# Kernel optimization log

Hardware: AMD Instinct MI355X
Metric: run time of the kernel (lower is better)

## Reference

```python
import jax, jax.numpy as jnp
import numpy as np

N, B, FIN, E, EDIM, H, C = 20000, 2, 256, 320000, 64, 8, 32


def setup_inputs() -> dict:
    key = jax.random.key(0)
    ks = jax.random.split(key, 12)
    s = 1.0 / np.sqrt(FIN)
    se = 1.0 / np.sqrt(EDIM)
    return {
        "x": jax.random.normal(ks[0], (N, B, FIN), jnp.float32),
        "edata": jax.random.normal(ks[1], (E, EDIM), jnp.float32),
        "edge_src": jax.random.randint(ks[2], (E,), 0, N, jnp.int32),
        "edge_dst": jax.random.randint(ks[3], (E,), 0, N, jnp.int32),
        "Wq": jax.random.normal(ks[4], (FIN, H * C), jnp.float32) * s,
        "bq": jnp.zeros((H * C,), jnp.float32),
        "Wk": jax.random.normal(ks[5], (FIN, H * C), jnp.float32) * s,
        "bk": jnp.zeros((H * C,), jnp.float32),
        "Wv": jax.random.normal(ks[6], (FIN, H * C), jnp.float32) * s,
        "bv": jnp.zeros((H * C,), jnp.float32),
        "We": jax.random.normal(ks[7], (EDIM, H * C), jnp.float32) * se,
        "Wr": jax.random.normal(ks[8], (FIN, H * C), jnp.float32) * s,
        "br": jnp.zeros((H * C,), jnp.float32),
    }


def reference(x, edata, edge_src, edge_dst, Wq, bq, Wk, bk, Wv, bv, We, Wr, br):
    # x: [N, B, FIN]; edata: [E, EDIM]
    q = (x @ Wq + bq).reshape(N, B, H, C)   # dst queries
    k = (x @ Wk + bk).reshape(N, B, H, C)   # src keys
    v = (x @ Wv + bv).reshape(N, B, H, C)   # src values
    e = (edata @ We).reshape(E, 1, H, C)    # edge feats, broadcast over batch

    scale = 1.0 / np.sqrt(C)
    # per-edge logits: (u_mul_v / sqrt(C) + edata).sum(-1) -> [E, B, H]
    logits = (k[edge_src] * q[edge_dst] * scale + e).sum(-1)

    # edge_softmax over edges sharing the same destination node
    m = jax.ops.segment_max(logits, edge_dst, num_segments=N)      # [N, B, H]
    ex = jnp.exp(logits - m[edge_dst])
    z = jax.ops.segment_sum(ex, edge_dst, num_segments=N)          # [N, B, H]
    alpha = ex / z[edge_dst]                                       # [E, B, H]

    # weighted scatter-sum aggregation: u_mul_e + sum over dst
    att_v = v[edge_src] * alpha[..., None]                         # [E, B, H, C]
    agg = jax.ops.segment_sum(att_v, edge_dst, num_segments=N)     # [N, B, H, C]

    out = agg.reshape(N, B, H * C) + (x @ Wr + br)
    return out
```

## Files before the change

### kernel.cpp

```cpp
#include <hip/hip_runtime.h>
#include <hip/hip_bf16.h>

#define NN    20000
#define BB    2
#define EE    320000
#define MROWS (NN * BB)

typedef __bf16 bf16x8 __attribute__((ext_vector_type(8)));
typedef float  floatx4 __attribute__((ext_vector_type(4)));


__global__ __launch_bounds__(256) void transpose_weights(
    const float* __restrict__ Wq, const float* __restrict__ Wk,
    const float* __restrict__ Wv, const float* __restrict__ Wr,
    __hip_bfloat16* __restrict__ wt) {
  __shared__ float TA[32][65];
  __shared__ float TB[32][65];
  int bt = blockIdx.x;
  const float *A, *B;
  int c0, jbase;
  if (bt < 8) { A = Wk; B = Wv; c0 = 32 * bt;      jbase = 64 * bt; }
  else        { A = Wq; B = Wr; c0 = 32 * (bt-8);  jbase = 512 + 64 * (bt-8); }
  int t = threadIdx.x;
  int krow = t >> 2;
  int cc = (t & 3) * 8;
  int sel = t >> 7;
  int u = t & 127;
  int ci = u >> 2;
  int kk0 = (u & 3) * 16;

  for (int kt = 0; kt < 4; ++kt) {
    int k = kt * 64 + krow;
    float4 a0 = *(const float4*)(A + (size_t)k * 256 + c0 + cc);
    float4 a1 = *(const float4*)(A + (size_t)k * 256 + c0 + cc + 4);
    float4 b0 = *(const float4*)(B + (size_t)k * 256 + c0 + cc);
    float4 b1 = *(const float4*)(B + (size_t)k * 256 + c0 + cc + 4);
    __syncthreads();
    TA[cc+0][krow]=a0.x; TA[cc+1][krow]=a0.y; TA[cc+2][krow]=a0.z; TA[cc+3][krow]=a0.w;
    TA[cc+4][krow]=a1.x; TA[cc+5][krow]=a1.y; TA[cc+6][krow]=a1.z; TA[cc+7][krow]=a1.w;
    TB[cc+0][krow]=b0.x; TB[cc+1][krow]=b0.y; TB[cc+2][krow]=b0.z; TB[cc+3][krow]=b0.w;
    TB[cc+4][krow]=b1.x; TB[cc+5][krow]=b1.y; TB[cc+6][krow]=b1.z; TB[cc+7][krow]=b1.w;
    __syncthreads();
    float (*T)[65] = sel ? TB : TA;
    int j = jbase + 2 * ci + sel;
    __hip_bfloat16* dst = wt + (size_t)j * 256 + kt * 64 + kk0;
    #pragma unroll
    for (int q = 0; q < 16; ++q) dst[q] = __float2bfloat16(T[ci][kk0 + q]);
  }
}

__global__ void prep_bias(const float* __restrict__ bq, const float* __restrict__ bk,
                          const float* __restrict__ bv, const float* __restrict__ br,
                          float* __restrict__ bcat) {
  int j = blockIdx.x * 256 + threadIdx.x;
  float val;
  if (j < 512) { int c = j >> 1;         val = (j & 1) ? bv[c] : bk[c]; }
  else         { int c = (j - 512) >> 1; val = (j & 1) ? br[c] : bq[c]; }
  bcat[j] = val;
}

__global__ void prep_wesum(const float* __restrict__ We, float* __restrict__ wesum) {
  int i = threadIdx.x;
  int h = i >> 6, d = i & 63;
  float s = 0.f;
  for (int c = 0; c < 32; ++c) s += We[(size_t)d * 256 + h * 32 + c];
  wesum[h * 64 + d] = s;
}

__global__ void zero_ints(int* __restrict__ p, int n) {
  int i = blockIdx.x * 256 + threadIdx.x;
  if (i < n) p[i] = 0;
}

__global__ void hist_kernel(const int* __restrict__ dst, int* __restrict__ counts) {
  int e = blockIdx.x * 256 + threadIdx.x;
  if (e < EE) atomicAdd(&counts[dst[e]], 1);
}

__global__ void scan_kernel(const int* __restrict__ counts,
                            int* __restrict__ offsets,
                            int* __restrict__ cursor) {
  __shared__ int part[256];
  int t = threadIdx.x;
  const int per = (NN + 255) / 256;
  int lo = t * per, hi = min(lo + per, NN);
  int s = 0;
  for (int i = lo; i < hi; ++i) s += counts[i];
  part[t] = s;
  __syncthreads();
  for (int off = 1; off < 256; off <<= 1) {
    int v = (t >= off) ? part[t - off] : 0;
    __syncthreads();
    part[t] += v;
    __syncthreads();
  }
  int base = (t == 0) ? 0 : part[t - 1];
  for (int i = lo; i < hi; ++i) {
    offsets[i] = base;
    cursor[i] = base;
    base += counts[i];
  }
  if (t == 255) offsets[NN] = base;
}

__global__ void scatter_kernel(const int* __restrict__ dst,
                               const int* __restrict__ src,
                               int* __restrict__ cursor,
                               int* __restrict__ ssrc,
                               int* __restrict__ pos) {
  int e = blockIdx.x * 256 + threadIdx.x;
  if (e < EE) {
    int p = atomicAdd(&cursor[dst[e]], 1);
    ssrc[p] = src[e];
    pos[e] = p;
  }
}

__global__ __launch_bounds__(256) void fused_gemm_esum(
    const float* __restrict__ x,
    const __bf16* __restrict__ wt,
    const float* __restrict__ bcat,
    __hip_bfloat16* __restrict__ outq,
    const float* __restrict__ edata,
    const float* __restrict__ wesum,
    const int* __restrict__ pos,
    float* __restrict__ esum) {
  const int LSTR = 40;
  __shared__ __attribute__((aligned(16))) __bf16 ABs[(64 + 256) * LSTR];
  int bid = blockIdx.x;
  int t = threadIdx.x;
  int g = bid / 3, rsub = bid - g * 3;

  if (rsub < 2) {
    int gb = g * 2 + rsub;
    __bf16* As = ABs;
    __bf16* Bs = ABs + 64 * LSTR;
    int m0 = (gb >> 2) * 64;
    int n0 = (gb & 3) * 256;
    int w = t >> 6, l = t & 63;
    int lr = l & 15, lq = l >> 4;
    int ar = t >> 2, ac = (t & 3) * 8;

    floatx4 acc[4][4] = {};

    for (int ks = 0; ks < 8; ++ks) {
      const float* xp = x + (size_t)(m0 + ar) * 256 + ks * 32 + ac;
      float4 f0 = *(const float4*)xp;
      float4 f1 = *(const float4*)(xp + 4);
      bf16x8 av;
      av[0] = (__bf16)f0.x; av[1] = (__bf16)f0.y;
      av[2] = (__bf16)f0.z; av[3] = (__bf16)f0.w;
      av[4] = (__bf16)f1.x; av[5] = (__bf16)f1.y;
      av[6] = (__bf16)f1.z; av[7] = (__bf16)f1.w;
      const __bf16* wp = wt + (size_t)(n0 + t) * 256 + ks * 32;
      bf16x8 b0 = *(const bf16x8*)(wp);
      bf16x8 b1 = *(const bf16x8*)(wp + 8);
      bf16x8 b2 = *(const bf16x8*)(wp + 16);
      bf16x8 b3 = *(const bf16x8*)(wp + 24);
      __syncthreads();
      *(bf16x8*)&As[ar * LSTR + ac] = av;
      __bf16* bsr = &Bs[t * LSTR];
      *(bf16x8*)(bsr)      = b0;
      *(bf16x8*)(bsr + 8)  = b1;
      *(bf16x8*)(bsr + 16) = b2;
      *(bf16x8*)(bsr + 24) = b3;
      __syncthreads();
      bf16x8 af[4], bf_[4];
      #pragma unroll
      for (int mt = 0; mt < 4; ++mt)
        af[mt] = *(const bf16x8*)&As[(16 * mt + lr) * LSTR + lq * 8];
      #pragma unroll
      for (int nt = 0; nt < 4; ++nt)
        bf_[nt] = *(const bf16x8*)&Bs[(64 * w + 16 * nt + lr) * LSTR + lq * 8];
      #pragma unroll
      for (int mt = 0; mt < 4; ++mt)
        #pragma unroll
        for (int nt = 0; nt < 4; ++nt)
          acc[mt][nt] = __builtin_amdgcn_mfma_f32_16x16x32_bf16(af[mt], bf_[nt], acc[mt][nt], 0, 0, 0);
    }

    #pragma unroll
    for (int mt = 0; mt < 4; ++mt)
      #pragma unroll
      for (int nt = 0; nt < 4; ++nt)
        #pragma unroll
        for (int r = 0; r < 4; ++r) {
          int gr = m0 + 16 * mt + lq * 4 + r;
          int gc = n0 + 64 * w + 16 * nt + lr;
          outq[(size_t)gr * 1024 + gc] = __float2bfloat16(acc[mt][nt][r] + bcat[gc]);
        }
  } else {
    float* wl = (float*)ABs;
    wl[t] = wesum[t];
    wl[t + 256] = wesum[t + 256];
    __syncthreads();
    int e = g * 256 + t;
    float acc[8] = {};
    const float* row = edata + (size_t)e * 64;
    for (int d = 0; d < 64; d += 4) {
      float4 v = *(const float4*)(row + d);
      #pragma unroll
      for (int hh = 0; hh < 8; ++hh) {
        const float* wv = &wl[hh * 64 + d];
        acc[hh] += v.x * wv[0] + v.y * wv[1] + v.z * wv[2] + v.w * wv[3];
      }
    }
    float* op = esum + (size_t)pos[e] * 8;
    *(float4*)op       = make_float4(acc[0], acc[1], acc[2], acc[3]);
    *(float4*)(op + 4) = make_float4(acc[4], acc[5], acc[6], acc[7]);
  }
}

__global__ __launch_bounds__(256) void aggregate_kernel(
    const unsigned int* __restrict__ qkvr,
    const float* __restrict__ esum,
    const int* __restrict__ offsets,
    const int* __restrict__ ssrc,
    float* __restrict__ out) {
  int t = threadIdx.x;
  int w = t >> 6, l = t & 63;
  int n = blockIdx.x * 4 + w;
  int h = l >> 3;
  int beg = offsets[n], end = offsets[n + 1];

  uint4 qra = *(const uint4*)(qkvr + (size_t)(2 * n) * 512 + 256 + l * 4);
  uint4 qrb = *(const uint4*)(qkvr + (size_t)(2 * n + 1) * 512 + 256 + l * 4);
  float qa0 = __uint_as_float(qra.x << 16), qa1 = __uint_as_float(qra.y << 16);
  float qa2 = __uint_as_float(qra.z << 16), qa3 = __uint_as_float(qra.w << 16);
  float qb0 = __uint_as_float(qrb.x << 16), qb1 = __uint_as_float(qrb.y << 16);
  float qb2 = __uint_as_float(qrb.z << 16), qb3 = __uint_as_float(qrb.w << 16);

  const unsigned* kvl = qkvr + l * 4;

  float za = 0.f, zb = 0.f;
  float aa0 = 0.f, aa1 = 0.f, aa2 = 0.f, aa3 = 0.f;
  float ab0 = 0.f, ab1 = 0.f, ab2 = 0.f, ab3 = 0.f;

  for (int base = beg; base < end; base += 64) {
    int chunk = min(64, end - base);
    int s_l = (l < chunk) ? ssrc[base + l] : 0;
    const float* esp = esum + (size_t)base * 8 + h;
    uint4 kA0 = {0,0,0,0}, kA1 = {0,0,0,0};
    uint4 kB0 = {0,0,0,0}, kB1 = {0,0,0,0};
    float eA = 0.f, eB = 0.f;
    {
      int s0 = __builtin_amdgcn_readlane(s_l, 0);
      const unsigned* p = kvl + (size_t)s0 * 1024;
      kA0 = *(const uint4*)p;
      kA1 = *(const uint4*)(p + 512);
      eA = esp[0];
    }
    if (chunk > 1) {
      int s1 = __builtin_amdgcn_readlane(s_l, 1);
      const unsigned* p = kvl + (size_t)s1 * 1024;
      kB0 = *(const uint4*)p;
      kB1 = *(const uint4*)(p + 512);
      eB = esp[8];
    }
    for (int i = 0; i < chunk; ++i) {
      uint4 k0 = kA0, k1 = kA1; float es = eA;
      kA0 = kB0; kA1 = kB1; eA = eB;
      if (i + 2 < chunk) {
        int s2 = __builtin_amdgcn_readlane(s_l, i + 2);
        const unsigned* p = kvl + (size_t)s2 * 1024;
        kB0 = *(const uint4*)p;
        kB1 = *(const uint4*)(p + 512);
        eB = esp[(size_t)(i + 2) * 8];
      }
      float pa = __uint_as_float(k0.x << 16) * qa0
               + __uint_as_float(k0.y << 16) * qa1
               + __uint_as_float(k0.z << 16) * qa2
               + __uint_as_float(k0.w << 16) * qa3;
      float pb = __uint_as_float(k1.x << 16) * qb0
               + __uint_as_float(k1.y << 16) * qb1
               + __uint_as_float(k1.z << 16) * qb2
               + __uint_as_float(k1.w << 16) * qb3;
      pa += __shfl_xor(pa, 1, 64);  pb += __shfl_xor(pb, 1, 64);
      pa += __shfl_xor(pa, 2, 64);  pb += __shfl_xor(pb, 2, 64);
      pa += __shfl_xor(pa, 4, 64);  pb += __shfl_xor(pb, 4, 64);
      float ea_ = __expf(pa * 0.17677669529663687f + es);
      float eb_ = __expf(pb * 0.17677669529663687f + es);
      za += ea_; zb += eb_;
      aa0 += ea_ * __uint_as_float(k0.x & 0xFFFF0000u);
      aa1 += ea_ * __uint_as_float(k0.y & 0xFFFF0000u);
      aa2 += ea_ * __uint_as_float(k0.z & 0xFFFF0000u);
      aa3 += ea_ * __uint_as_float(k0.w & 0xFFFF0000u);
      ab0 += eb_ * __uint_as_float(k1.x & 0xFFFF0000u);
      ab1 += eb_ * __uint_as_float(k1.y & 0xFFFF0000u);
      ab2 += eb_ * __uint_as_float(k1.z & 0xFFFF0000u);
      ab3 += eb_ * __uint_as_float(k1.w & 0xFFFF0000u);
    }
  }
  float ia = (za > 0.f) ? 1.f / za : 0.f;
  float ib = (zb > 0.f) ? 1.f / zb : 0.f;
  float4 oa = make_float4(aa0 * ia + __uint_as_float(qra.x & 0xFFFF0000u),
                          aa1 * ia + __uint_as_float(qra.y & 0xFFFF0000u),
                          aa2 * ia + __uint_as_float(qra.z & 0xFFFF0000u),
                          aa3 * ia + __uint_as_float(qra.w & 0xFFFF0000u));
  float4 ob = make_float4(ab0 * ib + __uint_as_float(qrb.x & 0xFFFF0000u),
                          ab1 * ib + __uint_as_float(qrb.y & 0xFFFF0000u),
                          ab2 * ib + __uint_as_float(qrb.z & 0xFFFF0000u),
                          ab3 * ib + __uint_as_float(qrb.w & 0xFFFF0000u));
  *(float4*)(out + (size_t)(2 * n) * 256 + l * 4) = oa;
  *(float4*)(out + (size_t)(2 * n + 1) * 256 + l * 4) = ob;
}

extern "C" void kernel_launch(void* const* d_in, const int* in_sizes, int n_in,
                              void* d_out, int out_size, void* d_ws, size_t ws_size,
                              hipStream_t stream) {
  (void)in_sizes; (void)n_in; (void)out_size; (void)ws_size;
  const float* x     = (const float*)d_in[0];
  const float* edata = (const float*)d_in[1];
  const int* esrc    = (const int*)d_in[2];
  const int* edst    = (const int*)d_in[3];
  const float* Wq    = (const float*)d_in[4];
  const float* bq    = (const float*)d_in[5];
  const float* Wk    = (const float*)d_in[6];
  const float* bk    = (const float*)d_in[7];
  const float* Wv    = (const float*)d_in[8];
  const float* bv    = (const float*)d_in[9];
  const float* We    = (const float*)d_in[10];
  const float* Wr    = (const float*)d_in[11];
  const float* br    = (const float*)d_in[12];
  float* out = (float*)d_out;

  char* ws = (char*)d_ws;
  size_t off = 0;
  auto carve = [&](size_t bytes) -> void* {
    void* p = ws + off;
    off += (bytes + 255) & ~(size_t)255;
    return p;
  };
  int* counts    = (int*)carve((size_t)NN * 4);
  int* offsets   = (int*)carve((size_t)(NN + 1) * 4);
  int* cursor    = (int*)carve((size_t)NN * 4);
  int* ssrc      = (int*)carve((size_t)EE * 4);
  int* pos       = (int*)carve((size_t)EE * 4);
  __hip_bfloat16* wt = (__hip_bfloat16*)carve((size_t)1024 * 256 * 2);
  float* bcat    = (float*)carve(1024 * 4);
  float* wesum   = (float*)carve(8 * 64 * 4);
  float* esum    = (float*)carve((size_t)EE * 8 * 4);
  __hip_bfloat16* qkvr = (__hip_bfloat16*)carve((size_t)MROWS * 1024 * 2);

  zero_ints<<<(NN + 255) / 256, 256, 0, stream>>>(counts, NN);
  transpose_weights<<<16, 256, 0, stream>>>(Wq, Wk, Wv, Wr, wt);
  prep_bias<<<4, 256, 0, stream>>>(bq, bk, bv, br, bcat);
  prep_wesum<<<1, 512, 0, stream>>>(We, wesum);
  hist_kernel<<<(EE + 255) / 256, 256, 0, stream>>>(edst, counts);
  scan_kernel<<<1, 256, 0, stream>>>(counts, offsets, cursor);
  scatter_kernel<<<(EE + 255) / 256, 256, 0, stream>>>(edst, esrc, cursor, ssrc, pos);
  fused_gemm_esum<<<3750, 256, 0, stream>>>(x, (const __bf16*)wt, bcat, qkvr,
                                            edata, wesum, pos, esum);
  aggregate_kernel<<<NN / 4, 256, 0, stream>>>((const unsigned int*)qkvr, esum,
                                               offsets, ssrc, out);
}
```

Measured before the change: 448.5 us.

## Merge prep kernels, fuse edge-sum into scatter, deepen aggregate prefetch

Folds the weight transpose, bias concat, We row-sum and histogram into one prep kernel, and replaces the zeroing kernel with a memset. The edge-feature reduction moves into the scatter kernel, which writes straight to the sorted position, so the pos array and its round trip go away. The GEMM becomes its own 2D-grid kernel. The aggregate loop now prefetches four neighbour rows instead of two to hide gather latency, at the cost of more registers and possibly lower occupancy.

```diff
diff --git a/kernel.cpp b/kernel.cpp
--- a/kernel.cpp
+++ b/kernel.cpp
@@ -10,71 +10,71 @@
 typedef float  floatx4 __attribute__((ext_vector_type(4)));
 
 
-__global__ __launch_bounds__(256) void transpose_weights(
+__global__ __launch_bounds__(256) void prep_kernel(
     const float* __restrict__ Wq, const float* __restrict__ Wk,
     const float* __restrict__ Wv, const float* __restrict__ Wr,
-    __hip_bfloat16* __restrict__ wt) {
+    __hip_bfloat16* __restrict__ wt,
+    const float* __restrict__ bq, const float* __restrict__ bk,
+    const float* __restrict__ bv, const float* __restrict__ br,
+    float* __restrict__ bcat,
+    const float* __restrict__ We, float* __restrict__ wesum,
+    const int* __restrict__ edst, int* __restrict__ counts) {
   __shared__ float TA[32][65];
   __shared__ float TB[32][65];
   int bt = blockIdx.x;
-  const float *A, *B;
-  int c0, jbase;
-  if (bt < 8) { A = Wk; B = Wv; c0 = 32 * bt;      jbase = 64 * bt; }
-  else        { A = Wq; B = Wr; c0 = 32 * (bt-8);  jbase = 512 + 64 * (bt-8); }
-  int t = threadIdx.x;
-  int krow = t >> 2;
-  int cc = (t & 3) * 8;
-  int sel = t >> 7;
-  int u = t & 127;
-  int ci = u >> 2;
-  int kk0 = (u & 3) * 16;
-
-  for (int kt = 0; kt < 4; ++kt) {
-    int k = kt * 64 + krow;
-    float4 a0 = *(const float4*)(A + (size_t)k * 256 + c0 + cc);
-    float4 a1 = *(const float4*)(A + (size_t)k * 256 + c0 + cc + 4);
-    float4 b0 = *(const float4*)(B + (size_t)k * 256 + c0 + cc);
-    float4 b1 = *(const float4*)(B + (size_t)k * 256 + c0 + cc + 4);
-    __syncthreads();
-    TA[cc+0][krow]=a0.x; TA[cc+1][krow]=a0.y; TA[cc+2][krow]=a0.z; TA[cc+3][krow]=a0.w;
-    TA[cc+4][krow]=a1.x; TA[cc+5][krow]=a1.y; TA[cc+6][krow]=a1.z; TA[cc+7][krow]=a1.w;
-    TB[cc+0][krow]=b0.x; TB[cc+1][krow]=b0.y; TB[cc+2][krow]=b0.z; TB[cc+3][krow]=b0.w;
-    TB[cc+4][krow]=b1.x; TB[cc+5][krow]=b1.y; TB[cc+6][krow]=b1.z; TB[cc+7][krow]=b1.w;
-    __syncthreads();
-    float (*T)[65] = sel ? TB : TA;
-    int j = jbase + 2 * ci + sel;
-    __hip_bfloat16* dst = wt + (size_t)j * 256 + kt * 64 + kk0;
-    #pragma unroll
-    for (int q = 0; q < 16; ++q) dst[q] = __float2bfloat16(T[ci][kk0 + q]);
-  }
-}
-
-__global__ void prep_bias(const float* __restrict__ bq, const float* __restrict__ bk,
-                          const float* __restrict__ bv, const float* __restrict__ br,
-                          float* __restrict__ bcat) {
-  int j = blockIdx.x * 256 + threadIdx.x;
-  float val;
-  if (j < 512) { int c = j >> 1;         val = (j & 1) ? bv[c] : bk[c]; }
-  else         { int c = (j - 512) >> 1; val = (j & 1) ? br[c] : bq[c]; }
-  bcat[j] = val;
-}
-
-__global__ void prep_wesum(const float* __restrict__ We, float* __restrict__ wesum) {
-  int i = threadIdx.x;
-  int h = i >> 6, d = i & 63;
-  float s = 0.f;
-  for (int c = 0; c < 32; ++c) s += We[(size_t)d * 256 + h * 32 + c];
-  wesum[h * 64 + d] = s;
-}
-
-__global__ void zero_ints(int* __restrict__ p, int n) {
-  int i = blockIdx.x * 256 + threadIdx.x;
-  if (i < n) p[i] = 0;
-}
-
-__global__ void hist_kernel(const int* __restrict__ dst, int* __restrict__ counts) {
-  int e = blockIdx.x * 256 + threadIdx.x;
-  if (e < EE) atomicAdd(&counts[dst[e]], 1);
+  int t = threadIdx.x;
+
+  if (bt < 16) {
+    const float *A, *B;
+    int c0, jbase;
+    if (bt < 8) { A = Wk; B = Wv; c0 = 32 * bt;      jbase = 64 * bt; }
+    else        { A = Wq; B = Wr; c0 = 32 * (bt-8);  jbase = 512 + 64 * (bt-8); }
+    int krow = t >> 2;
+    int cc = (t & 3) * 8;
+    int sel = t >> 7;
+    int u = t & 127;
+    int ci = u >> 2;
+    int kk0 = (u & 3) * 16;
+
+    for (int kt = 0; kt < 4; ++kt) {
+      int k = kt * 64 + krow;
+      float4 a0 = *(const float4*)(A + (size_t)k * 256 + c0 + cc);
+      float4 a1 = *(const float4*)(A + (size_t)k * 256 + c0 + cc + 4);
+      float4 b0 = *(const float4*)(B + (size_t)k * 256 + c0 + cc);
+      float4 b1 = *(const float4*)(B + (size_t)k * 256 + c0 + cc + 4);
+      __syncthreads();
+      TA[cc+0][krow]=a0.x; TA[cc+1][krow]=a0.y; TA[cc+2][krow]=a0.z; TA[cc+3][krow]=a0.w;
+      TA[cc+4][krow]=a1.x; TA[cc+5][krow]=a1.y; TA[cc+6][krow]=a1.z; TA[cc+7][krow]=a1.w;
+      TB[cc+0][krow]=b0.x; TB[cc+1][krow]=b0.y; TB[cc+2][krow]=b0.z; TB[cc+3][krow]=b0.w;
+      TB[cc+4][krow]=b1.x; TB[cc+5][krow]=b1.y; TB[cc+6][krow]=b1.z; TB[cc+7][krow]=b1.w;
+      __syncthreads();
+      float (*T)[65] = sel ? TB : TA;
+      int j = jbase + 2 * ci + sel;
+      __hip_bfloat16* dst = wt + (size_t)j * 256 + kt * 64 + kk0;
+      #pragma unroll
+      for (int q = 0; q < 16; ++q) dst[q] = __float2bfloat16(T[ci][kk0 + q]);
+    }
+  } else if (bt == 16) {
+    #pragma unroll
+    for (int jj = 0; jj < 4; ++jj) {
+      int j = jj * 256 + t;
+      float val;
+      if (j < 512) { int c = j >> 1;         val = (j & 1) ? bv[c] : bk[c]; }
+      else         { int c = (j - 512) >> 1; val = (j & 1) ? br[c] : bq[c]; }
+      bcat[j] = val;
+    }
+    #pragma unroll
+    for (int ii = 0; ii < 2; ++ii) {
+      int i = ii * 256 + t;
+      int h = i >> 6, d = i & 63;
+      float s = 0.f;
+      for (int c = 0; c < 32; ++c) s += We[(size_t)d * 256 + h * 32 + c];
+      wesum[h * 64 + d] = s;
+    }
+  } else {
+    int e = (bt - 17) * 256 + t;
+    if (e < EE) atomicAdd(&counts[edst[e]], 1);
+  }
 }
 
 __global__ void scan_kernel(const int* __restrict__ counts,
@@ -85,6 +85,7 @@
   const int per = (NN + 255) / 256;
   int lo = t * per, hi = min(lo + per, NN);
   int s = 0;
+  #pragma unroll 4
   for (int i = lo; i < hi; ++i) s += counts[i];
   part[t] = s;
   __syncthreads();
@@ -103,113 +104,130 @@
   if (t == 255) offsets[NN] = base;
 }
 
-__global__ void scatter_kernel(const int* __restrict__ dst,
-                               const int* __restrict__ src,
-                               int* __restrict__ cursor,
-                               int* __restrict__ ssrc,
-                               int* __restrict__ pos) {
-  int e = blockIdx.x * 256 + threadIdx.x;
-  if (e < EE) {
-    int p = atomicAdd(&cursor[dst[e]], 1);
-    ssrc[p] = src[e];
-    pos[e] = p;
-  }
-}
-
-__global__ __launch_bounds__(256) void fused_gemm_esum(
+__global__ __launch_bounds__(256) void scatter_esum(
+    const int* __restrict__ edst, const int* __restrict__ esrc,
+    int* __restrict__ cursor,
+    const float* __restrict__ edata, const float* __restrict__ wesum,
+    int* __restrict__ ssrc, float* __restrict__ esum) {
+  __shared__ float wl[512];
+  int t = threadIdx.x;
+  wl[t] = wesum[t];
+  wl[t + 256] = wesum[t + 256];
+  __syncthreads();
+  int e = blockIdx.x * 256 + t;
+  int p = atomicAdd(&cursor[edst[e]], 1);
+  ssrc[p] = esrc[e];
+  float acc[8] = {};
+  const float* row = edata + (size_t)e * 64;
+  for (int d = 0; d < 64; d += 4) {
+    float4 v = *(const float4*)(row + d);
+    #pragma unroll
+    for (int hh = 0; hh < 8; ++hh) {
+      const float* wv = &wl[hh * 64 + d];
+      acc[hh] += v.x * wv[0] + v.y * wv[1] + v.z * wv[2] + v.w * wv[3];
+    }
+  }
+  float* op = esum + (size_t)p * 8;
+  *(float4*)op       = make_float4(acc[0], acc[1], acc[2], acc[3]);
+  *(float4*)(op + 4) = make_float4(acc[4], acc[5], acc[6], acc[7]);
+}
+
+__global__ __launch_bounds__(256) void gemm_qkvr(
     const float* __restrict__ x,
     const __bf16* __restrict__ wt,
     const float* __restrict__ bcat,
-    __hip_bfloat16* __restrict__ outq,
-    const float* __restrict__ edata,
-    const float* __restrict__ wesum,
-    const int* __restrict__ pos,
-    float* __restrict__ esum) {
+    __hip_bfloat16* __restrict__ out) {
   const int LSTR = 40;
-  __shared__ __attribute__((aligned(16))) __bf16 ABs[(64 + 256) * LSTR];
-  int bid = blockIdx.x;
-  int t = threadIdx.x;
-  int g = bid / 3, rsub = bid - g * 3;
-
-  if (rsub < 2) {
-    int gb = g * 2 + rsub;
-    __bf16* As = ABs;
-    __bf16* Bs = ABs + 64 * LSTR;
-    int m0 = (gb >> 2) * 64;
-    int n0 = (gb & 3) * 256;
-    int w = t >> 6, l = t & 63;
-    int lr = l & 15, lq = l >> 4;
-    int ar = t >> 2, ac = (t & 3) * 8;
-
-    floatx4 acc[4][4] = {};
-
-    for (int ks = 0; ks < 8; ++ks) {
-      const float* xp = x + (size_t)(m0 + ar) * 256 + ks * 32 + ac;
-      float4 f0 = *(const float4*)xp;
-      float4 f1 = *(const float4*)(xp + 4);
-      bf16x8 av;
-      av[0] = (__bf16)f0.x; av[1] = (__bf16)f0.y;
-      av[2] = (__bf16)f0.z; av[3] = (__bf16)f0.w;
-      av[4] = (__bf16)f1.x; av[5] = (__bf16)f1.y;
-      av[6] = (__bf16)f1.z; av[7] = (__bf16)f1.w;
-      const __bf16* wp = wt + (size_t)(n0 + t) * 256 + ks * 32;
-      bf16x8 b0 = *(const bf16x8*)(wp);
-      bf16x8 b1 = *(const bf16x8*)(wp + 8);
-      bf16x8 b2 = *(const bf16x8*)(wp + 16);
-      bf16x8 b3 = *(const bf16x8*)(wp + 24);
-      __syncthreads();
-      *(bf16x8*)&As[ar * LSTR + ac] = av;
-      __bf16* bsr = &Bs[t * LSTR];
-      *(bf16x8*)(bsr)      = b0;
-      *(bf16x8*)(bsr + 8)  = b1;
-      *(bf16x8*)(bsr + 16) = b2;
-      *(bf16x8*)(bsr + 24) = b3;
-      __syncthreads();
-      bf16x8 af[4], bf_[4];
-      #pragma unroll
-      for (int mt = 0; mt < 4; ++mt)
-        af[mt] = *(const bf16x8*)&As[(16 * mt + lr) * LSTR + lq * 8];
-      #pragma unroll
-      for (int nt = 0; nt < 4; ++nt)
-        bf_[nt] = *(const bf16x8*)&Bs[(64 * w + 16 * nt + lr) * LSTR + lq * 8];
-      #pragma unroll
-      for (int mt = 0; mt < 4; ++mt)
-        #pragma unroll
-        for (int nt = 0; nt < 4; ++nt)
-          acc[mt][nt] = __builtin_amdgcn_mfma_f32_16x16x32_bf16(af[mt], bf_[nt], acc[mt][nt], 0, 0, 0);
-    }
-
+  __shared__ __attribute__((aligned(16))) __bf16 As[64 * LSTR];
+  __shared__ __attribute__((aligned(16))) __bf16 Bs[256 * LSTR];
+
+  int m0 = blockIdx.y * 64;
+  int n0 = blockIdx.x * 256;
+  int t = threadIdx.x;
+  int w = t >> 6, l = t & 63;
+  int lr = l & 15, lq = l >> 4;
+  int ar = t >> 2, ac = (t & 3) * 8;
+
+  floatx4 acc[4][4] = {};
+
+  for (int ks = 0; ks < 8; ++ks) {
+    const float* xp = x + (size_t)(m0 + ar) * 256 + ks * 32 + ac;
+    float4 f0 = *(const float4*)xp;
+    float4 f1 = *(const float4*)(xp + 4);
+    bf16x8 av;
+    av[0] = (__bf16)f0.x; av[1] = (__bf16)f0.y;
+    av[2] = (__bf16)f0.z; av[3] = (__bf16)f0.w;
+    av[4] = (__bf16)f1.x; av[5] = (__bf16)f1.y;
+    av[6] = (__bf16)f1.z; av[7] = (__bf16)f1.w;
+    const __bf16* wp = wt + (size_t)(n0 + t) * 256 + ks * 32;
+    bf16x8 b0 = *(const bf16x8*)(wp);
+    bf16x8 b1 = *(const bf16x8*)(wp + 8);
+    bf16x8 b2 = *(const bf16x8*)(wp + 16);
+    bf16x8 b3 = *(const bf16x8*)(wp + 24);
+    __syncthreads();
+    *(bf16x8*)&As[ar * LSTR + ac] = av;
+    __bf16* bsr = &Bs[t * LSTR];
+    *(bf16x8*)(bsr)      = b0;
+    *(bf16x8*)(bsr + 8)  = b1;
+    *(bf16x8*)(bsr + 16) = b2;
+    *(bf16x8*)(bsr + 24) = b3;
+    __syncthreads();
+    bf16x8 af[4], bf_[4];
+    #pragma unroll
+    for (int mt = 0; mt < 4; ++mt)
+      af[mt] = *(const bf16x8*)&As[(16 * mt + lr) * LSTR + lq * 8];
+    #pragma unroll
+    for (int nt = 0; nt < 4; ++nt)
+      bf_[nt] = *(const bf16x8*)&Bs[(64 * w + 16 * nt + lr) * LSTR + lq * 8];
     #pragma unroll
     for (int mt = 0; mt < 4; ++mt)
       #pragma unroll
       for (int nt = 0; nt < 4; ++nt)
-        #pragma unroll
-        for (int r = 0; r < 4; ++r) {
-          int gr = m0 + 16 * mt + lq * 4 + r;
-          int gc = n0 + 64 * w + 16 * nt + lr;
-          outq[(size_t)gr * 1024 + gc] = __float2bfloat16(acc[mt][nt][r] + bcat[gc]);
-        }
-  } else {
-    float* wl = (float*)ABs;
-    wl[t] = wesum[t];
-    wl[t + 256] = wesum[t + 256];
-    __syncthreads();
-    int e = g * 256 + t;
-    float acc[8] = {};
-    const float* row = edata + (size_t)e * 64;
-    for (int d = 0; d < 64; d += 4) {
-      float4 v = *(const float4*)(row + d);
+        acc[mt][nt] = __builtin_amdgcn_mfma_f32_16x16x32_bf16(af[mt], bf_[nt], acc[mt][nt], 0, 0, 0);
+  }
+
+  #pragma unroll
+  for (int mt = 0; mt < 4; ++mt)
+    #pragma unroll
+    for (int nt = 0; nt < 4; ++nt)
       #pragma unroll
-      for (int hh = 0; hh < 8; ++hh) {
-        const float* wv = &wl[hh * 64 + d];
-        acc[hh] += v.x * wv[0] + v.y * wv[1] + v.z * wv[2] + v.w * wv[3];
+      for (int r = 0; r < 4; ++r) {
+        int gr = m0 + 16 * mt + lq * 4 + r;
+        int gc = n0 + 64 * w + 16 * nt + lr;
+        out[(size_t)gr * 1024 + gc] = __float2bfloat16(acc[mt][nt][r] + bcat[gc]);
       }
-    }
-    float* op = esum + (size_t)pos[e] * 8;
-    *(float4*)op       = make_float4(acc[0], acc[1], acc[2], acc[3]);
-    *(float4*)(op + 4) = make_float4(acc[4], acc[5], acc[6], acc[7]);
-  }
-}
+}
+
+#define LOADSLOT(K0, K1, EV, IDX)                                    \
+  { int s_ = __builtin_amdgcn_readlane(s_l, (IDX));                  \
+    const unsigned* p_ = kvl + (size_t)s_ * 1024;                    \
+    K0 = *(const uint4*)p_;                                          \
+    K1 = *(const uint4*)(p_ + 512);                                  \
+    EV = esp[(size_t)(IDX) * 8]; }
+
+#define CONSUME(K0, K1, EV)                                          \
+  { float pa = __uint_as_float(K0.x << 16) * qa0                     \
+             + __uint_as_float(K0.y << 16) * qa1                     \
+             + __uint_as_float(K0.z << 16) * qa2                     \
+             + __uint_as_float(K0.w << 16) * qa3;                    \
+    float pb = __uint_as_float(K1.x << 16) * qb0                     \
+             + __uint_as_float(K1.y << 16) * qb1                     \
+             + __uint_as_float(K1.z << 16) * qb2                     \
+             + __uint_as_float(K1.w << 16) * qb3;                    \
+    pa += __shfl_xor(pa, 1, 64);  pb += __shfl_xor(pb, 1, 64);       \
+    pa += __shfl_xor(pa, 2, 64);  pb += __shfl_xor(pb, 2, 64);       \
+    pa += __shfl_xor(pa, 4, 64);  pb += __shfl_xor(pb, 4, 64);       \
+    float ea_ = __expf(pa * 0.17677669529663687f + EV);              \
+    float eb_ = __expf(pb * 0.17677669529663687f + EV);              \
+    za += ea_; zb += eb_;                                            \
+    aa0 += ea_ * __uint_as_float(K0.x & 0xFFFF0000u);                \
+    aa1 += ea_ * __uint_as_float(K0.y & 0xFFFF0000u);                \
+    aa2 += ea_ * __uint_as_float(K0.z & 0xFFFF0000u);                \
+    aa3 += ea_ * __uint_as_float(K0.w & 0xFFFF0000u);                \
+    ab0 += eb_ * __uint_as_float(K1.x & 0xFFFF0000u);                \
+    ab1 += eb_ * __uint_as_float(K1.y & 0xFFFF0000u);                \
+    ab2 += eb_ * __uint_as_float(K1.z & 0xFFFF0000u);                \
+    ab3 += eb_ * __uint_as_float(K1.w & 0xFFFF0000u); }
 
 __global__ __launch_bounds__(256) void aggregate_kernel(
     const unsigned int* __restrict__ qkvr,
@@ -240,55 +258,28 @@
     int chunk = min(64, end - base);
     int s_l = (l < chunk) ? ssrc[base + l] : 0;
     const float* esp = esum + (size_t)base * 8 + h;
-    uint4 kA0 = {0,0,0,0}, kA1 = {0,0,0,0};
-    uint4 kB0 = {0,0,0,0}, kB1 = {0,0,0,0};
-    float eA = 0.f, eB = 0.f;
-    {
-      int s0 = __builtin_amdgcn_readlane(s_l, 0);
-      const unsigned* p = kvl + (size_t)s0 * 1024;
-      kA0 = *(const uint4*)p;
-      kA1 = *(const uint4*)(p + 512);
-      eA = esp[0];
-    }
-    if (chunk > 1) {
-      int s1 = __builtin_amdgcn_readlane(s_l, 1);
-      const unsigned* p = kvl + (size_t)s1 * 1024;
-      kB0 = *(const uint4*)p;
-      kB1 = *(const uint4*)(p + 512);
-      eB = esp[8];
-    }
-    for (int i = 0; i < chunk; ++i) {
-      uint4 k0 = kA0, k1 = kA1; float es = eA;
-      kA0 = kB0; kA1 = kB1; eA = eB;
-      if (i + 2 < chunk) {
-        int s2 = __builtin_amdgcn_readlane(s_l, i + 2);
-        const unsigned* p = kvl + (size_t)s2 * 1024;
-        kB0 = *(const uint4*)p;
-        kB1 = *(const uint4*)(p + 512);
-        eB = esp[(size_t)(i + 2) * 8];
+    uint4 kA0 = {0,0,0,0}, kA1 = {0,0,0,0}, kB0 = {0,0,0,0}, kB1 = {0,0,0,0};
+    uint4 kC0 = {0,0,0,0}, kC1 = {0,0,0,0}, kD0 = {0,0,0,0}, kD1 = {0,0,0,0};
+    float eA = 0.f, eB = 0.f, eC = 0.f, eD = 0.f;
+    LOADSLOT(kA0, kA1, eA, 0);
+    if (chunk > 1) LOADSLOT(kB0, kB1, eB, 1);
+    if (chunk > 2) LOADSLOT(kC0, kC1, eC, 2);
+    if (chunk > 3) LOADSLOT(kD0, kD1, eD, 3);
+    for (int i = 0; i < chunk; i += 4) {
+      CONSUME(kA0, kA1, eA);
+      if (i + 4 < chunk) LOADSLOT(kA0, kA1, eA, i + 4);
+      if (i + 1 < chunk) {
+        CONSUME(kB0, kB1, eB);
+        if (i + 5 < chunk) LOADSLOT(kB0, kB1, eB, i + 5);
+        if (i + 2 < chunk) {
+          CONSUME(kC0, kC1, eC);
+          if (i + 6 < chunk) LOADSLOT(kC0, kC1, eC, i + 6);
+          if (i + 3 < chunk) {
+            CONSUME(kD0, kD1, eD);
+            if (i + 7 < chunk) LOADSLOT(kD0, kD1, eD, i + 7);
+          }
+        }
       }
-      float pa = __uint_as_float(k0.x << 16) * qa0
-               + __uint_as_float(k0.y << 16) * qa1
-               + __uint_as_float(k0.z << 16) * qa2
-               + __uint_as_float(k0.w << 16) * qa3;
-      float pb = __uint_as_float(k1.x << 16) * qb0
-               + __uint_as_float(k1.y << 16) * qb1
-               + __uint_as_float(k1.z << 16) * qb2
-               + __uint_as_float(k1.w << 16) * qb3;
-      pa += __shfl_xor(pa, 1, 64);  pb += __shfl_xor(pb, 1, 64);
-      pa += __shfl_xor(pa, 2, 64);  pb += __shfl_xor(pb, 2, 64);
-      pa += __shfl_xor(pa, 4, 64);  pb += __shfl_xor(pb, 4, 64);
-      float ea_ = __expf(pa * 0.17677669529663687f + es);
-      float eb_ = __expf(pb * 0.17677669529663687f + es);
-      za += ea_; zb += eb_;
-      aa0 += ea_ * __uint_as_float(k0.x & 0xFFFF0000u);
-      aa1 += ea_ * __uint_as_float(k0.y & 0xFFFF0000u);
-      aa2 += ea_ * __uint_as_float(k0.z & 0xFFFF0000u);
-      aa3 += ea_ * __uint_as_float(k0.w & 0xFFFF0000u);
-      ab0 += eb_ * __uint_as_float(k1.x & 0xFFFF0000u);
-      ab1 += eb_ * __uint_as_float(k1.y & 0xFFFF0000u);
-      ab2 += eb_ * __uint_as_float(k1.z & 0xFFFF0000u);
-      ab3 += eb_ * __uint_as_float(k1.w & 0xFFFF0000u);
     }
   }
   float ia = (za > 0.f) ? 1.f / za : 0.f;
@@ -335,22 +326,19 @@
   int* offsets   = (int*)carve((size_t)(NN + 1) * 4);
   int* cursor    = (int*)carve((size_t)NN * 4);
   int* ssrc      = (int*)carve((size_t)EE * 4);
-  int* pos       = (int*)carve((size_t)EE * 4);
   __hip_bfloat16* wt = (__hip_bfloat16*)carve((size_t)1024 * 256 * 2);
   float* bcat    = (float*)carve(1024 * 4);
   float* wesum   = (float*)carve(8 * 64 * 4);
   float* esum    = (float*)carve((size_t)EE * 8 * 4);
   __hip_bfloat16* qkvr = (__hip_bfloat16*)carve((size_t)MROWS * 1024 * 2);
 
-  zero_ints<<<(NN + 255) / 256, 256, 0, stream>>>(counts, NN);
-  transpose_weights<<<16, 256, 0, stream>>>(Wq, Wk, Wv, Wr, wt);
-  prep_bias<<<4, 256, 0, stream>>>(bq, bk, bv, br, bcat);
-  prep_wesum<<<1, 512, 0, stream>>>(We, wesum);
-  hist_kernel<<<(EE + 255) / 256, 256, 0, stream>>>(edst, counts);
+  hipMemsetAsync(counts, 0, (size_t)NN * 4, stream);
+  prep_kernel<<<17 + (EE + 255) / 256, 256, 0, stream>>>(
+      Wq, Wk, Wv, Wr, wt, bq, bk, bv, br, bcat, We, wesum, edst, counts);
   scan_kernel<<<1, 256, 0, stream>>>(counts, offsets, cursor);
-  scatter_kernel<<<(EE + 255) / 256, 256, 0, stream>>>(edst, esrc, cursor, ssrc, pos);
-  fused_gemm_esum<<<3750, 256, 0, stream>>>(x, (const __bf16*)wt, bcat, qkvr,
-                                            edata, wesum, pos, esum);
+  scatter_esum<<<EE / 256, 256, 0, stream>>>(edst, esrc, cursor, edata, wesum,
+                                             ssrc, esum);
+  gemm_qkvr<<<dim3(4, 625), 256, 0, stream>>>(x, (const __bf16*)wt, bcat, qkvr);
   aggregate_kernel<<<NN / 4, 256, 0, stream>>>((const unsigned int*)qkvr, esum,
                                                offsets, ssrc, out);
 }
```

Result: faster. 428.0 us (-4.6%).
